# Performance work log

Hardware: AMD Instinct MI355X
Metric: run time of the kernel (lower is better)

Reference implementation:

```python
import jax, jax.numpy as jnp
import numpy as np

B, S, D_IN, D_OUT = 4, 2048, 1024, 1024


def setup_inputs() -> dict:
    key = jax.random.key(0)
    ks = jax.random.split(key, 7)
    s_in = 1.0 / np.sqrt(D_IN)
    return {
        "x": jax.random.normal(ks[0], (B, S, D_IN), dtype=jnp.float32),
        "Wq": jax.random.uniform(ks[1], (D_IN, D_OUT), jnp.float32, -s_in, s_in),
        "bq": jax.random.uniform(ks[2], (D_OUT,), jnp.float32, -s_in, s_in),
        "Wk": jax.random.uniform(ks[3], (D_IN, D_OUT), jnp.float32, -s_in, s_in),
        "bk": jax.random.uniform(ks[4], (D_OUT,), jnp.float32, -s_in, s_in),
        "Wv": jax.random.uniform(ks[5], (D_IN, D_OUT), jnp.float32, -s_in, s_in),
        "bv": jax.random.uniform(ks[6], (D_OUT,), jnp.float32, -s_in, s_in),
    }


def reference(x, Wq, bq, Wk, bk, Wv, bv):
    # q,k,v: [B, S, D_OUT]
    q = jnp.einsum("bsd,de->bse", x, Wq) + bq
    k = jnp.einsum("bsd,de->bse", x, Wk) + bk
    v = jnp.einsum("bsd,de->bse", x, Wv) + bv
    scale = 1.0 / jnp.sqrt(jnp.asarray(q.shape[-1], q.dtype))
    scores = jnp.einsum("bqe,bke->bqk", q, k) * scale  # [B, S, S]
    attn = jax.nn.softmax(scores, axis=-1)
    return jnp.einsum("bqk,bke->bqe", attn, v)
```

## Files before the change

kernel.cpp:

```cpp
#include <hip/hip_runtime.h>
#include <hip/hip_bf16.h>
#include <stdint.h>


#define Bsz 4
#define Ssz 2048
#define Dsz 1024

typedef __attribute__((ext_vector_type(8))) short short8;
typedef __attribute__((ext_vector_type(4))) float floatx4;
typedef const __attribute__((address_space(1))) void* gptr_t;
typedef __attribute__((address_space(3))) void* lptr_t;

__device__ __forceinline__ ushort f32_to_bf16(float f) {
    union { float f; uint32_t u; } c; c.f = f;
    uint32_t u = c.u;
    u += 0x7fffu + ((u >> 16) & 1u);
    return (ushort)(u >> 16);
}

__global__ __launch_bounds__(256, 2) void k_qkv(
    const ushort* __restrict__ xb, const ushort* __restrict__ Wt,
    const float* __restrict__ bq, const float* __restrict__ bk,
    const float* __restrict__ bv, ushort* __restrict__ QKV,
    ushort* __restrict__ Vt)
{
    __shared__ ushort lsA[2][128 * 32];
    __shared__ ushort lsB[2][3][128 * 32];

    const int tid  = threadIdx.x;
    const int bx   = blockIdx.x;
    const int by   = blockIdx.y;
    const int row0 = by * 128;
    const int col0 = bx * 128;

    const int lane = tid & 63;
    const int wave = tid >> 6;
    const int wr   = (wave >> 1) * 64;
    const int wc   = (wave & 1) * 64;
    const int m16  = lane & 15;
    const int quad = lane >> 4;

    floatx4 acc[3][4][4];
#pragma unroll
    for (int z = 0; z < 3; z++)
#pragma unroll
        for (int i = 0; i < 4; i++)
#pragma unroll
            for (int j = 0; j < 4; j++) acc[z][i][j] = (floatx4){0.f, 0.f, 0.f, 0.f};

    const int srow = tid >> 2;
    const int skc  = (tid & 3) ^ ((srow >> 1) & 3);
    const ushort* ga = xb + (size_t)(row0 + srow) * Dsz + skc * 8;
    const ushort* gb0 = Wt + (size_t)(col0 + srow) * Dsz + skc * 8;

    const int aoff = (quad ^ ((m16 >> 1) & 3)) * 8;

    __builtin_amdgcn_global_load_lds((gptr_t)(ga),                    (lptr_t)(lsA[0] + tid * 8),        16, 0, 0);
    __builtin_amdgcn_global_load_lds((gptr_t)(ga + (size_t)64 * Dsz), (lptr_t)(lsA[0] + 2048 + tid * 8), 16, 0, 0);
#pragma unroll
    for (int z = 0; z < 3; z++) {
        const ushort* gb = gb0 + (size_t)z * Dsz * Dsz;
        __builtin_amdgcn_global_load_lds((gptr_t)(gb),                    (lptr_t)(lsB[0][z] + tid * 8),        16, 0, 0);
        __builtin_amdgcn_global_load_lds((gptr_t)(gb + (size_t)64 * Dsz), (lptr_t)(lsB[0][z] + 2048 + tid * 8), 16, 0, 0);
    }

    for (int k0 = 0; k0 < Dsz; k0 += 32) {
        const int cur = (k0 >> 5) & 1;
        __syncthreads();
        if (k0 + 32 < Dsz) {
            const int nxt = cur ^ 1;
            const int kn = k0 + 32;
            __builtin_amdgcn_global_load_lds((gptr_t)(ga + kn),                    (lptr_t)(lsA[nxt] + tid * 8),        16, 0, 0);
            __builtin_amdgcn_global_load_lds((gptr_t)(ga + kn + (size_t)64 * Dsz), (lptr_t)(lsA[nxt] + 2048 + tid * 8), 16, 0, 0);
#pragma unroll
            for (int z = 0; z < 3; z++) {
                const ushort* gb = gb0 + (size_t)z * Dsz * Dsz + kn;
                __builtin_amdgcn_global_load_lds((gptr_t)(gb),                    (lptr_t)(lsB[nxt][z] + tid * 8),        16, 0, 0);
                __builtin_amdgcn_global_load_lds((gptr_t)(gb + (size_t)64 * Dsz), (lptr_t)(lsB[nxt][z] + 2048 + tid * 8), 16, 0, 0);
            }
        }

        short8 af[4];
#pragma unroll
        for (int mi = 0; mi < 4; mi++)
            af[mi] = *(const short8*)&lsA[cur][(wr + mi * 16 + m16) * 32 + aoff];
#pragma unroll
        for (int z = 0; z < 3; z++) {
            short8 bfr[4];
#pragma unroll
            for (int ni = 0; ni < 4; ni++)
                bfr[ni] = *(const short8*)&lsB[cur][z][(wc + ni * 16 + m16) * 32 + aoff];
#pragma unroll
            for (int mi = 0; mi < 4; mi++)
#pragma unroll
                for (int ni = 0; ni < 4; ni++)
                    acc[z][mi][ni] = __builtin_amdgcn_mfma_f32_16x16x32_bf16(af[mi], bfr[ni], acc[z][mi][ni], 0, 0, 0);
        }
    }

#pragma unroll
    for (int ni = 0; ni < 4; ni++) {
        const int gcol = col0 + wc + ni * 16 + m16;
        const float bqv = bq[gcol], bkv = bk[gcol], bvv = bv[gcol];
#pragma unroll
        for (int mi = 0; mi < 4; mi++) {
            const int grow0 = row0 + wr + mi * 16 + quad * 4;
            ushort4 vpack;
#pragma unroll
            for (int j = 0; j < 4; j++) {
                QKV[(size_t)(grow0 + j) * Dsz + gcol] = f32_to_bf16((acc[0][mi][ni][j] + bqv) * 0.03125f);
                QKV[(size_t)(Bsz * Ssz) * Dsz + (size_t)(grow0 + j) * Dsz + gcol] = f32_to_bf16(acc[1][mi][ni][j] + bkv);
                const ushort vv = f32_to_bf16(acc[2][mi][ni][j] + bvv);
                if (j == 0) vpack.x = vv; else if (j == 1) vpack.y = vv;
                else if (j == 2) vpack.z = vv; else vpack.w = vv;
            }
            const int batch = grow0 >> 11;
            const int s0 = grow0 & (Ssz - 1);
            *(ushort4*)&Vt[(size_t)batch * Dsz * Ssz + (size_t)gcol * Ssz + s0] = vpack;
        }
    }
}

template <bool OUT_BF16>
__device__ __forceinline__ void gemm128(
    int bx, int by,
    const ushort* __restrict__ A, int lda,
    const ushort* __restrict__ Bt, int ldb,
    int K,
    void* __restrict__ Cout, int ldc,
    const float* __restrict__ bias, float alpha)
{
    __shared__ ushort lsA[2][128 * 32];
    __shared__ ushort lsB[2][128 * 32];

    const int tid  = threadIdx.x;
    const int row0 = by * 128;
    const int col0 = bx * 128;

    const int lane = tid & 63;
    const int wave = tid >> 6;
    const int wr   = (wave >> 1) * 64;
    const int wc   = (wave & 1) * 64;
    const int m16  = lane & 15;
    const int quad = lane >> 4;

    floatx4 acc[4][4];
#pragma unroll
    for (int i = 0; i < 4; i++)
#pragma unroll
        for (int j = 0; j < 4; j++) acc[i][j] = (floatx4){0.f, 0.f, 0.f, 0.f};

    const int srow = tid >> 2;
    const int skc  = (tid & 3) ^ ((srow >> 1) & 3);
    const ushort* ga = A  + (size_t)(row0 + srow) * lda + skc * 8;
    const ushort* gb = Bt + (size_t)(col0 + srow) * ldb + skc * 8;
    const int aoff = (quad ^ ((m16 >> 1) & 3)) * 8;

    __builtin_amdgcn_global_load_lds((gptr_t)(ga),                     (lptr_t)(lsA[0] + tid * 8),        16, 0, 0);
    __builtin_amdgcn_global_load_lds((gptr_t)(ga + (size_t)64 * lda), (lptr_t)(lsA[0] + 2048 + tid * 8), 16, 0, 0);
    __builtin_amdgcn_global_load_lds((gptr_t)(gb),                     (lptr_t)(lsB[0] + tid * 8),        16, 0, 0);
    __builtin_amdgcn_global_load_lds((gptr_t)(gb + (size_t)64 * ldb), (lptr_t)(lsB[0] + 2048 + tid * 8), 16, 0, 0);

    for (int k0 = 0; k0 < K; k0 += 32) {
        const int cur = (k0 >> 5) & 1;
        __syncthreads();
        if (k0 + 32 < K) {
            const int nxt = cur ^ 1;
            const int kn = k0 + 32;
            __builtin_amdgcn_global_load_lds((gptr_t)(ga + kn),                     (lptr_t)(lsA[nxt] + tid * 8),        16, 0, 0);
            __builtin_amdgcn_global_load_lds((gptr_t)(ga + kn + (size_t)64 * lda), (lptr_t)(lsA[nxt] + 2048 + tid * 8), 16, 0, 0);
            __builtin_amdgcn_global_load_lds((gptr_t)(gb + kn),                     (lptr_t)(lsB[nxt] + tid * 8),        16, 0, 0);
            __builtin_amdgcn_global_load_lds((gptr_t)(gb + kn + (size_t)64 * ldb), (lptr_t)(lsB[nxt] + 2048 + tid * 8), 16, 0, 0);
        }

        short8 af[4], bfr[4];
#pragma unroll
        for (int mi = 0; mi < 4; mi++)
            af[mi] = *(const short8*)&lsA[cur][(wr + mi * 16 + m16) * 32 + aoff];
#pragma unroll
        for (int ni = 0; ni < 4; ni++)
            bfr[ni] = *(const short8*)&lsB[cur][(wc + ni * 16 + m16) * 32 + aoff];
#pragma unroll
        for (int mi = 0; mi < 4; mi++)
#pragma unroll
            for (int ni = 0; ni < 4; ni++)
                acc[mi][ni] = __builtin_amdgcn_mfma_f32_16x16x32_bf16(af[mi], bfr[ni], acc[mi][ni], 0, 0, 0);
    }

#pragma unroll
    for (int ni = 0; ni < 4; ni++) {
        const int gcol = col0 + wc + ni * 16 + m16;
        const float bv = bias ? bias[gcol] : 0.0f;
#pragma unroll
        for (int mi = 0; mi < 4; mi++) {
            const int grow0 = row0 + wr + mi * 16 + quad * 4;
#pragma unroll
            for (int j = 0; j < 4; j++) {
                float v = (acc[mi][ni][j] + bv) * alpha;
                if (OUT_BF16)
                    ((ushort*)Cout)[(size_t)(grow0 + j) * ldc + gcol] = f32_to_bf16(v);
                else
                    ((float*)Cout)[(size_t)(grow0 + j) * ldc + gcol] = v;
            }
        }
    }
}

__global__ __launch_bounds__(256) void k_cvt_x(const float* __restrict__ x, ushort* __restrict__ xb) {
    int i = (blockIdx.x * 256 + threadIdx.x) * 4;
    float4 v = *(const float4*)(x + i);
    ushort4 o;
    o.x = f32_to_bf16(v.x); o.y = f32_to_bf16(v.y);
    o.z = f32_to_bf16(v.z); o.w = f32_to_bf16(v.w);
    *(ushort4*)(xb + i) = o;
}

__global__ __launch_bounds__(256) void k_wt(const float* __restrict__ Wq, const float* __restrict__ Wk,
                                            const float* __restrict__ Wv, ushort* __restrict__ Wt) {
    __shared__ float tile[32][33];
    const int z = blockIdx.z;
    const float* W = (z == 0) ? Wq : ((z == 1) ? Wk : Wv);
    ushort* out = Wt + (size_t)z * Dsz * Dsz;
    const int kb = blockIdx.y * 32, nb = blockIdx.x * 32;
    const int tx = threadIdx.x, ty = threadIdx.y;
#pragma unroll
    for (int j = 0; j < 32; j += 8)
        tile[ty + j][tx] = W[(size_t)(kb + ty + j) * Dsz + nb + tx];
    __syncthreads();
#pragma unroll
    for (int j = 0; j < 32; j += 8)
        out[(size_t)(nb + ty + j) * Dsz + kb + tx] = f32_to_bf16(tile[tx][ty + j]);
}

__global__ __launch_bounds__(256) void k_scores(const ushort* __restrict__ QKV, float* __restrict__ scores) {
    const int b = blockIdx.z;
    const int lin = blockIdx.y * 16 + blockIdx.x;
    const int c = lin & 7, m = lin >> 3;
    const int by = 2 * c + (m & 1);
    const int bx = m >> 1;
    const ushort* Q = QKV + (size_t)b * Ssz * Dsz;
    const ushort* Kb = QKV + (size_t)(Bsz + b) * Ssz * Dsz;
    gemm128<false>(bx, by, Q, Dsz, Kb, Dsz, Dsz, scores + (size_t)b * Ssz * Ssz, Ssz, nullptr, 1.0f);
}

__global__ __launch_bounds__(256) void k_softmax(float* __restrict__ scores) {
    const size_t row = blockIdx.x;
    float* rp = scores + row * Ssz;
    const int tid = threadIdx.x;
    float4 v0 = ((const float4*)rp)[tid];
    float4 v1 = ((const float4*)rp)[tid + 256];
    float m = fmaxf(fmaxf(fmaxf(v0.x, v0.y), fmaxf(v0.z, v0.w)),
                    fmaxf(fmaxf(v1.x, v1.y), fmaxf(v1.z, v1.w)));
#pragma unroll
    for (int o = 32; o > 0; o >>= 1) m = fmaxf(m, __shfl_down(m, o, 64));
    __shared__ float redm[4];
    if ((tid & 63) == 0) redm[tid >> 6] = m;
    __syncthreads();
    const float rm = fmaxf(fmaxf(redm[0], redm[1]), fmaxf(redm[2], redm[3]));
    v0.x = __expf(v0.x - rm); v0.y = __expf(v0.y - rm);
    v0.z = __expf(v0.z - rm); v0.w = __expf(v0.w - rm);
    v1.x = __expf(v1.x - rm); v1.y = __expf(v1.y - rm);
    v1.z = __expf(v1.z - rm); v1.w = __expf(v1.w - rm);
    float s = v0.x + v0.y + v0.z + v0.w + v1.x + v1.y + v1.z + v1.w;
#pragma unroll
    for (int o = 32; o > 0; o >>= 1) s += __shfl_down(s, o, 64);
    __shared__ float reds[4];
    if ((tid & 63) == 0) reds[tid >> 6] = s;
    __syncthreads();
    const float inv = 1.0f / (reds[0] + reds[1] + reds[2] + reds[3]);
    ushort4 o0, o1;
    o0.x = f32_to_bf16(v0.x * inv); o0.y = f32_to_bf16(v0.y * inv);
    o0.z = f32_to_bf16(v0.z * inv); o0.w = f32_to_bf16(v0.w * inv);
    o1.x = f32_to_bf16(v1.x * inv); o1.y = f32_to_bf16(v1.y * inv);
    o1.z = f32_to_bf16(v1.z * inv); o1.w = f32_to_bf16(v1.w * inv);
    ((ushort4*)rp)[tid] = o0;
    ((ushort4*)rp)[tid + 256] = o1;
}

__global__ __launch_bounds__(256) void k_pv(const float* __restrict__ scores, const ushort* __restrict__ Vt,
                                            float* __restrict__ out) {
    const int b = blockIdx.z;
    const int lin = blockIdx.y * 8 + blockIdx.x;
    const int c = lin & 7, m = lin >> 3;
    const int by = 2 * c + (m & 1);
    const int bx = m >> 1;
    const ushort* P = (const ushort*)(scores + (size_t)b * Ssz * Ssz);
    const ushort* Bt = Vt + (size_t)b * Dsz * Ssz;
    gemm128<false>(bx, by, P, 2 * Ssz, Bt, Ssz, Ssz, out + (size_t)b * Ssz * Dsz, Dsz, nullptr, 1.0f);
}

extern "C" void kernel_launch(void* const* d_in, const int* in_sizes, int n_in,
                              void* d_out, int out_size, void* d_ws, size_t ws_size,
                              hipStream_t stream) {
    const float* x  = (const float*)d_in[0];
    const float* Wq = (const float*)d_in[1];
    const float* bq = (const float*)d_in[2];
    const float* Wk = (const float*)d_in[3];
    const float* bk = (const float*)d_in[4];
    const float* Wv = (const float*)d_in[5];
    const float* bv = (const float*)d_in[6];
    float* out = (float*)d_out;

    char* ws = (char*)d_ws;
    ushort* xb     = (ushort*)(ws);
    ushort* Wt     = (ushort*)(ws + 16777216);
    ushort* QKV    = (ushort*)(ws + 23068672);
    ushort* Vt     = (ushort*)(ws + 73400320);
    float*  scores = (float*) (ws + 90177536);

    k_cvt_x<<<dim3(Bsz * Ssz * Dsz / (256 * 4)), dim3(256), 0, stream>>>(x, xb);
    k_wt<<<dim3(32, 32, 3), dim3(32, 8), 0, stream>>>(Wq, Wk, Wv, Wt);
    k_qkv<<<dim3(Dsz / 128, Bsz * Ssz / 128), dim3(256), 0, stream>>>(xb, Wt, bq, bk, bv, QKV, Vt);
    k_scores<<<dim3(Ssz / 128, Ssz / 128, Bsz), dim3(256), 0, stream>>>(QKV, scores);
    k_softmax<<<dim3(Bsz * Ssz), dim3(256), 0, stream>>>(scores);
    k_pv<<<dim3(Dsz / 128, Ssz / 128, Bsz), dim3(256), 0, stream>>>(scores, Vt, out);
}
```

Measured before the change: 277.8 us.

## Replace QKV and scores GEMMs with 256x256-tile, 8-wave pipelined core

Adds a shared 256x256x64 GEMM core with 512 threads, double-buffered direct global-to-LDS loads split into four staged pieces, raw barriers and MFMA priority bumps. The QKV projection and the QK^T scores kernels now use it, with XCD-aware block index remapping. The QKV kernel now treats Wq/Wk/Wv as one concatenated 3072-column matrix instead of computing three accumulators per tile. The goal is more data reuse per tile and better overlap of loads with MFMA work. In exchange, LDS and register use per block go up, and far fewer blocks are launched (384 and 256).

```diff
diff --git a/kernel.cpp b/kernel.cpp
--- a/kernel.cpp
+++ b/kernel.cpp
@@ -19,105 +19,254 @@
     return (ushort)(u >> 16);
 }
 
-__global__ __launch_bounds__(256, 2) void k_qkv(
+__device__ __forceinline__ void glds16(const ushort* g, ushort* l) {
+    __builtin_amdgcn_global_load_lds((gptr_t)g, (lptr_t)l, 16, 0, 0);
+}
+
+__device__ __forceinline__ void barrier_raw() {
+    asm volatile("" ::: "memory");
+    __builtin_amdgcn_s_barrier();
+    asm volatile("" ::: "memory");
+}
+
+#define MFMA_QUAD(MB, NB)                                                              \
+    _Pragma("unroll")                                                                  \
+    for (int m_ = 0; m_ < 4; m_++) {                                                   \
+        _Pragma("unroll")                                                              \
+        for (int n_ = 0; n_ < 2; n_++) {                                               \
+            acc[(MB) * 4 + m_][(NB) * 2 + n_] = __builtin_amdgcn_mfma_f32_16x16x32_bf16( \
+                af[m_][0], bf[(NB) * 2 + n_][0], acc[(MB) * 4 + m_][(NB) * 2 + n_], 0, 0, 0); \
+            acc[(MB) * 4 + m_][(NB) * 2 + n_] = __builtin_amdgcn_mfma_f32_16x16x32_bf16( \
+                af[m_][1], bf[(NB) * 2 + n_][1], acc[(MB) * 4 + m_][(NB) * 2 + n_], 0, 0, 0); \
+        }                                                                              \
+    }
+
+#define LOAD_A(half)                                                                   \
+    _Pragma("unroll")                                                                  \
+    for (int m_ = 0; m_ < 4; m_++) {                                                   \
+        af[m_][0] = *(const short8*)(lA + aBase + ((half) * 4 + m_) * 1024 + c0);      \
+        af[m_][1] = *(const short8*)(lA + aBase + ((half) * 4 + m_) * 1024 + c1);      \
+    }
+
+#define LOAD_B(pn)                                                                     \
+    _Pragma("unroll")                                                                  \
+    for (int n_ = 0; n_ < 2; n_++) {                                                   \
+        bf[(pn) * 2 + n_][0] = *(const short8*)(lB + bBase + ((pn) * 2 + n_) * 1024 + c0); \
+        bf[(pn) * 2 + n_][1] = *(const short8*)(lB + bBase + ((pn) * 2 + n_) * 1024 + c1); \
+    }
+
+template <int NT>
+__device__ __forceinline__ void gemm256_core(
+    const ushort* __restrict__ A, int lda,
+    const ushort* __restrict__ Bt, int ldb,
+    int row0, int col0, floatx4 (&acc)[8][4])
+{
+    __shared__ __align__(16) ushort lsA[2][256 * 64];
+    __shared__ __align__(16) ushort lsB[2][256 * 64];
+
+    const int tid  = threadIdx.x;
+    const int lane = tid & 63;
+    const int wave = tid >> 6;
+    const int wr   = (wave >> 2) * 128;
+    const int wc   = (wave & 3) * 64;
+    const int m16  = lane & 15;
+    const int quad = lane >> 4;
+
+#pragma unroll
+    for (int i = 0; i < 8; i++)
+#pragma unroll
+        for (int j = 0; j < 4; j++) acc[i][j] = (floatx4){0.f, 0.f, 0.f, 0.f};
+
+    const int sRow = tid >> 3;
+    const int sC   = ((tid & 7) ^ (sRow & 7)) * 8;
+    const ushort* aSrc = A  + (size_t)(row0 + sRow) * lda + sC;
+    const ushort* bSrc = Bt + (size_t)(col0 + sRow) * ldb + sC;
+    ushort* dA = &lsA[0][0] + tid * 8;
+    ushort* dB = &lsB[0][0] + tid * 8;
+
+    const int aBase = (wr + m16) * 64;
+    const int bBase = (wc + m16) * 64;
+    const int c0 = (quad ^ (m16 & 7)) * 8;
+    const int c1 = c0 ^ 32;
+
+    auto stage = [&](int kt, int buf, int pair) {
+        const size_t ko = (size_t)kt * 64;
+        const int bo = buf * 16384;
+        if (pair == 0) {
+            glds16(aSrc + ko,                      dA + bo);
+            glds16(aSrc + ko + (size_t)64 * lda,   dA + bo + 4096);
+        } else if (pair == 1) {
+            glds16(aSrc + ko + (size_t)128 * lda,  dA + bo + 8192);
+            glds16(aSrc + ko + (size_t)192 * lda,  dA + bo + 12288);
+        } else if (pair == 2) {
+            glds16(bSrc + ko,                      dB + bo);
+            glds16(bSrc + ko + (size_t)64 * ldb,   dB + bo + 4096);
+        } else {
+            glds16(bSrc + ko + (size_t)128 * ldb,  dB + bo + 8192);
+            glds16(bSrc + ko + (size_t)192 * ldb,  dB + bo + 12288);
+        }
+    };
+
+    stage(0, 0, 0); stage(0, 0, 1); stage(0, 0, 2); stage(0, 0, 3);
+    stage(1, 1, 0);
+    asm volatile("s_waitcnt vmcnt(2)" ::: "memory");
+    barrier_raw();
+
+    short8 af[4][2], bf[4][2];
+
+    for (int kt = 0; kt < NT; ++kt) {
+        const int buf = kt & 1;
+        const ushort* lA = &lsA[buf][0];
+        const ushort* lB = &lsB[buf][0];
+        const bool pf1 = (kt + 1 < NT);
+
+        LOAD_A(0);
+        LOAD_B(0);
+        if (pf1) stage(kt + 1, buf ^ 1, 1);
+        barrier_raw();
+        __builtin_amdgcn_s_setprio(1);
+        MFMA_QUAD(0, 0);
+        __builtin_amdgcn_s_setprio(0);
+        barrier_raw();
+
+        LOAD_B(1);
+        if (pf1) stage(kt + 1, buf ^ 1, 2);
+        barrier_raw();
+        __builtin_amdgcn_s_setprio(1);
+        MFMA_QUAD(0, 1);
+        __builtin_amdgcn_s_setprio(0);
+        barrier_raw();
+
+        LOAD_A(1);
+        if (pf1) stage(kt + 1, buf ^ 1, 3);
+        barrier_raw();
+        __builtin_amdgcn_s_setprio(1);
+        MFMA_QUAD(1, 0);
+        __builtin_amdgcn_s_setprio(0);
+        barrier_raw();
+
+        if (kt + 2 < NT) stage(kt + 2, buf, 0);
+        __builtin_amdgcn_s_setprio(1);
+        MFMA_QUAD(1, 1);
+        __builtin_amdgcn_s_setprio(0);
+        if (kt + 2 < NT)      { asm volatile("s_waitcnt vmcnt(2)" ::: "memory"); }
+        else if (kt + 1 < NT) { asm volatile("s_waitcnt vmcnt(0)" ::: "memory"); }
+        barrier_raw();
+    }
+}
+
+__global__ __launch_bounds__(512, 2) void k_qkv256(
     const ushort* __restrict__ xb, const ushort* __restrict__ Wt,
     const float* __restrict__ bq, const float* __restrict__ bk,
     const float* __restrict__ bv, ushort* __restrict__ QKV,
     ushort* __restrict__ Vt)
 {
-    __shared__ ushort lsA[2][128 * 32];
-    __shared__ ushort lsB[2][3][128 * 32];
+    const int bid = blockIdx.x;
+    const int wg  = (bid & 7) * 48 + (bid >> 3);
+    const int bm  = wg & 31;
+    const int bn  = wg >> 5;
+    const int row0  = bm * 256;
+    const int col0n = bn * 256;
+
+    floatx4 acc[8][4];
+    gemm256_core<16>(xb, Dsz, Wt, Dsz, row0, col0n, acc);
 
     const int tid  = threadIdx.x;
-    const int bx   = blockIdx.x;
-    const int by   = blockIdx.y;
-    const int row0 = by * 128;
-    const int col0 = bx * 128;
-
     const int lane = tid & 63;
     const int wave = tid >> 6;
-    const int wr   = (wave >> 1) * 64;
-    const int wc   = (wave & 1) * 64;
+    const int wr   = (wave >> 2) * 128;
+    const int wc   = (wave & 3) * 64;
     const int m16  = lane & 15;
     const int quad = lane >> 4;
 
-    floatx4 acc[3][4][4];
-#pragma unroll
-    for (int z = 0; z < 3; z++)
-#pragma unroll
-        for (int i = 0; i < 4; i++)
-#pragma unroll
-            for (int j = 0; j < 4; j++) acc[z][i][j] = (floatx4){0.f, 0.f, 0.f, 0.f};
-
-    const int srow = tid >> 2;
-    const int skc  = (tid & 3) ^ ((srow >> 1) & 3);
-    const ushort* ga = xb + (size_t)(row0 + srow) * Dsz + skc * 8;
-    const ushort* gb0 = Wt + (size_t)(col0 + srow) * Dsz + skc * 8;
-
-    const int aoff = (quad ^ ((m16 >> 1) & 3)) * 8;
-
-    __builtin_amdgcn_global_load_lds((gptr_t)(ga),                    (lptr_t)(lsA[0] + tid * 8),        16, 0, 0);
-    __builtin_amdgcn_global_load_lds((gptr_t)(ga + (size_t)64 * Dsz), (lptr_t)(lsA[0] + 2048 + tid * 8), 16, 0, 0);
-#pragma unroll
-    for (int z = 0; z < 3; z++) {
-        const ushort* gb = gb0 + (size_t)z * Dsz * Dsz;
-        __builtin_amdgcn_global_load_lds((gptr_t)(gb),                    (lptr_t)(lsB[0][z] + tid * 8),        16, 0, 0);
-        __builtin_amdgcn_global_load_lds((gptr_t)(gb + (size_t)64 * Dsz), (lptr_t)(lsB[0][z] + 2048 + tid * 8), 16, 0, 0);
-    }
-
-    for (int k0 = 0; k0 < Dsz; k0 += 32) {
-        const int cur = (k0 >> 5) & 1;
-        __syncthreads();
-        if (k0 + 32 < Dsz) {
-            const int nxt = cur ^ 1;
-            const int kn = k0 + 32;
-            __builtin_amdgcn_global_load_lds((gptr_t)(ga + kn),                    (lptr_t)(lsA[nxt] + tid * 8),        16, 0, 0);
-            __builtin_amdgcn_global_load_lds((gptr_t)(ga + kn + (size_t)64 * Dsz), (lptr_t)(lsA[nxt] + 2048 + tid * 8), 16, 0, 0);
-#pragma unroll
-            for (int z = 0; z < 3; z++) {
-                const ushort* gb = gb0 + (size_t)z * Dsz * Dsz + kn;
-                __builtin_amdgcn_global_load_lds((gptr_t)(gb),                    (lptr_t)(lsB[nxt][z] + tid * 8),        16, 0, 0);
-                __builtin_amdgcn_global_load_lds((gptr_t)(gb + (size_t)64 * Dsz), (lptr_t)(lsB[nxt][z] + 2048 + tid * 8), 16, 0, 0);
+    const int z     = bn >> 2;
+    const int colz0 = col0n & 1023;
+
+    if (z == 0) {
+#pragma unroll
+        for (int ni = 0; ni < 4; ni++) {
+            const int colz = colz0 + wc + ni * 16 + m16;
+            const float bqv = bq[colz];
+#pragma unroll
+            for (int mi = 0; mi < 8; mi++) {
+                const int grow0 = row0 + wr + mi * 16 + quad * 4;
+#pragma unroll
+                for (int j = 0; j < 4; j++)
+                    QKV[(size_t)(grow0 + j) * Dsz + colz] =
+                        f32_to_bf16((acc[mi][ni][j] + bqv) * 0.03125f);
             }
         }
-
-        short8 af[4];
-#pragma unroll
-        for (int mi = 0; mi < 4; mi++)
-            af[mi] = *(const short8*)&lsA[cur][(wr + mi * 16 + m16) * 32 + aoff];
-#pragma unroll
-        for (int z = 0; z < 3; z++) {
-            short8 bfr[4];
-#pragma unroll
-            for (int ni = 0; ni < 4; ni++)
-                bfr[ni] = *(const short8*)&lsB[cur][z][(wc + ni * 16 + m16) * 32 + aoff];
-#pragma unroll
-            for (int mi = 0; mi < 4; mi++)
-#pragma unroll
-                for (int ni = 0; ni < 4; ni++)
-                    acc[z][mi][ni] = __builtin_amdgcn_mfma_f32_16x16x32_bf16(af[mi], bfr[ni], acc[z][mi][ni], 0, 0, 0);
-        }
-    }
-
+    } else if (z == 1) {
+        ushort* Kout = QKV + (size_t)(Bsz * Ssz) * Dsz;
+#pragma unroll
+        for (int ni = 0; ni < 4; ni++) {
+            const int colz = colz0 + wc + ni * 16 + m16;
+            const float bkv = bk[colz];
+#pragma unroll
+            for (int mi = 0; mi < 8; mi++) {
+                const int grow0 = row0 + wr + mi * 16 + quad * 4;
+#pragma unroll
+                for (int j = 0; j < 4; j++)
+                    Kout[(size_t)(grow0 + j) * Dsz + colz] =
+                        f32_to_bf16(acc[mi][ni][j] + bkv);
+            }
+        }
+    } else {
+#pragma unroll
+        for (int ni = 0; ni < 4; ni++) {
+            const int colz = colz0 + wc + ni * 16 + m16;
+            const float bvv = bv[colz];
+#pragma unroll
+            for (int mi = 0; mi < 8; mi++) {
+                const int grow0 = row0 + wr + mi * 16 + quad * 4;
+                ushort4 vpack;
+                vpack.x = f32_to_bf16(acc[mi][ni][0] + bvv);
+                vpack.y = f32_to_bf16(acc[mi][ni][1] + bvv);
+                vpack.z = f32_to_bf16(acc[mi][ni][2] + bvv);
+                vpack.w = f32_to_bf16(acc[mi][ni][3] + bvv);
+                const int batch = grow0 >> 11;
+                const int s0 = grow0 & (Ssz - 1);
+                *(ushort4*)&Vt[(size_t)batch * Dsz * Ssz + (size_t)colz * Ssz + s0] = vpack;
+            }
+        }
+    }
+}
+
+__global__ __launch_bounds__(512, 2) void k_scores256(
+    const ushort* __restrict__ QKV, float* __restrict__ scores)
+{
+    const int bid = blockIdx.x;
+    const int wg  = (bid & 7) * 32 + (bid >> 3);
+    const int b   = wg >> 6;
+    const int bm  = (wg >> 3) & 7;
+    const int bn  = wg & 7;
+    const int row0 = bm * 256;
+    const int col0 = bn * 256;
+
+    const ushort* Q  = QKV + (size_t)b * Ssz * Dsz;
+    const ushort* Kb = QKV + (size_t)(Bsz + b) * Ssz * Dsz;
+
+    floatx4 acc[8][4];
+    gemm256_core<16>(Q, Dsz, Kb, Dsz, row0, col0, acc);
+
+    const int tid  = threadIdx.x;
+    const int lane = tid & 63;
+    const int wave = tid >> 6;
+    const int wr   = (wave >> 2) * 128;
+    const int wc   = (wave & 3) * 64;
+    const int m16  = lane & 15;
+    const int quad = lane >> 4;
+
+    float* out = scores + (size_t)b * Ssz * Ssz;
 #pragma unroll
     for (int ni = 0; ni < 4; ni++) {
         const int gcol = col0 + wc + ni * 16 + m16;
-        const float bqv = bq[gcol], bkv = bk[gcol], bvv = bv[gcol];
-#pragma unroll
-        for (int mi = 0; mi < 4; mi++) {
+#pragma unroll
+        for (int mi = 0; mi < 8; mi++) {
             const int grow0 = row0 + wr + mi * 16 + quad * 4;
-            ushort4 vpack;
-#pragma unroll
-            for (int j = 0; j < 4; j++) {
-                QKV[(size_t)(grow0 + j) * Dsz + gcol] = f32_to_bf16((acc[0][mi][ni][j] + bqv) * 0.03125f);
-                QKV[(size_t)(Bsz * Ssz) * Dsz + (size_t)(grow0 + j) * Dsz + gcol] = f32_to_bf16(acc[1][mi][ni][j] + bkv);
-                const ushort vv = f32_to_bf16(acc[2][mi][ni][j] + bvv);
-                if (j == 0) vpack.x = vv; else if (j == 1) vpack.y = vv;
-                else if (j == 2) vpack.z = vv; else vpack.w = vv;
-            }
-            const int batch = grow0 >> 11;
-            const int s0 = grow0 & (Ssz - 1);
-            *(ushort4*)&Vt[(size_t)batch * Dsz * Ssz + (size_t)gcol * Ssz + s0] = vpack;
+#pragma unroll
+            for (int j = 0; j < 4; j++)
+                out[(size_t)(grow0 + j) * Ssz + gcol] = acc[mi][ni][j];
         }
     }
 }
@@ -231,17 +380,6 @@
 #pragma unroll
     for (int j = 0; j < 32; j += 8)
         out[(size_t)(nb + ty + j) * Dsz + kb + tx] = f32_to_bf16(tile[tx][ty + j]);
-}
-
-__global__ __launch_bounds__(256) void k_scores(const ushort* __restrict__ QKV, float* __restrict__ scores) {
-    const int b = blockIdx.z;
-    const int lin = blockIdx.y * 16 + blockIdx.x;
-    const int c = lin & 7, m = lin >> 3;
-    const int by = 2 * c + (m & 1);
-    const int bx = m >> 1;
-    const ushort* Q = QKV + (size_t)b * Ssz * Dsz;
-    const ushort* Kb = QKV + (size_t)(Bsz + b) * Ssz * Dsz;
-    gemm128<false>(bx, by, Q, Dsz, Kb, Dsz, Dsz, scores + (size_t)b * Ssz * Ssz, Ssz, nullptr, 1.0f);
 }
 
 __global__ __launch_bounds__(256) void k_softmax(float* __restrict__ scores) {
@@ -311,8 +449,8 @@
 
     k_cvt_x<<<dim3(Bsz * Ssz * Dsz / (256 * 4)), dim3(256), 0, stream>>>(x, xb);
     k_wt<<<dim3(32, 32, 3), dim3(32, 8), 0, stream>>>(Wq, Wk, Wv, Wt);
-    k_qkv<<<dim3(Dsz / 128, Bsz * Ssz / 128), dim3(256), 0, stream>>>(xb, Wt, bq, bk, bv, QKV, Vt);
-    k_scores<<<dim3(Ssz / 128, Ssz / 128, Bsz), dim3(256), 0, stream>>>(QKV, scores);
+    k_qkv256<<<dim3(384), dim3(512), 0, stream>>>(xb, Wt, bq, bk, bv, QKV, Vt);
+    k_scores256<<<dim3(256), dim3(512), 0, stream>>>(QKV, scores);
     k_softmax<<<dim3(Bsz * Ssz), dim3(256), 0, stream>>>(scores);
     k_pv<<<dim3(Dsz / 128, Ssz / 128, Bsz), dim3(256), 0, stream>>>(scores, Vt, out);
 }
```

New measurement: 291.5 us. 4.9% more time.
